# Optimization experiments

Hardware: AMD Instinct MI355X
Metric: run time of the kernel (lower is better)

## Reference

```python
import jax, jax.numpy as jnp
import numpy as np

DIM = 1024
B, TI, TJ = 8, 2048, 2048
EPS = 1e-5


def layernorm(x, g, b):
    mu = jnp.mean(x, axis=-1, keepdims=True)
    var = jnp.var(x, axis=-1, keepdims=True)
    return (x - mu) * jax.lax.rsqrt(var + EPS) * g + b


def setup_inputs() -> dict:
    key = jax.random.key(0)
    ks = jax.random.split(key, 12)
    s = 1.0 / np.sqrt(DIM)
    return {
        "target": jax.random.normal(ks[0], (B, TI, DIM), jnp.float32),
        "source_k": jax.random.normal(ks[1], (B, TJ, DIM), jnp.float32),
        "source_v": jax.random.normal(ks[2], (B, TJ, DIM), jnp.float32),
        "Wq": jax.random.uniform(ks[3], (DIM, DIM), jnp.float32, -s, s),
        "bq": jax.random.uniform(ks[4], (DIM,), jnp.float32, -s, s),
        "Wk": jax.random.uniform(ks[5], (DIM, DIM), jnp.float32, -s, s),
        "bk": jax.random.uniform(ks[6], (DIM,), jnp.float32, -s, s),
        "Wv": jax.random.uniform(ks[7], (DIM, DIM), jnp.float32, -s, s),
        "bv": jax.random.uniform(ks[8], (DIM,), jnp.float32, -s, s),
        "g_t": jnp.ones((DIM,), jnp.float32),
        "b_t": jnp.zeros((DIM,), jnp.float32),
        "g_k": jnp.ones((DIM,), jnp.float32),
        "b_k": jnp.zeros((DIM,), jnp.float32),
        "g_v": jnp.ones((DIM,), jnp.float32),
        "b_v": jnp.zeros((DIM,), jnp.float32),
    }


def reference(target, source_k, source_v, Wq, bq, Wk, bk, Wv, bv,
              g_t, b_t, g_k, b_k, g_v, b_v):
    scale = DIM ** (-0.5)
    t = layernorm(target, g_t, b_t)
    sk = layernorm(source_k, g_k, b_k)
    sv = layernorm(source_v, g_v, b_v)
    # torch Linear: x @ W.T + b
    q = jnp.einsum('bid,ed->bie', t, Wq) + bq
    k = jnp.einsum('bjd,ed->bje', sk, Wk) + bk
    v = jnp.einsum('bjd,ed->bje', sv, Wv) + bv
    dots = jnp.einsum('bid,bjd->bij', q, k) * scale
    attn = jax.nn.softmax(dots, axis=2)
    return jnp.einsum('bij,bjd->bid', attn, v)
```

## Files before the change

kernel.cpp:

```cpp
#include <hip/hip_runtime.h>
#include <cstdint>

using u16 = unsigned short;
using u32 = unsigned int;
typedef __attribute__((ext_vector_type(8))) short short8;
typedef __attribute__((ext_vector_type(4))) float f32x4;

__device__ __forceinline__ float bf2f(u16 u) { return __uint_as_float(((u32)u) << 16); }
__device__ __forceinline__ u16 f2bf(float f) {
    u32 u = __float_as_uint(f);
    u32 r = u + 0x7fffu + ((u >> 16) & 1u);
    return (u16)(r >> 16);
}

__device__ __forceinline__ void load_lds16(const void* g, void* l) {
    __builtin_amdgcn_global_load_lds((const __attribute__((address_space(1))) void*)g,
                                     (__attribute__((address_space(3))) void*)l, 16, 0, 0);
}

__global__ __launch_bounds__(256)
void ln_cast_kernel(const float* __restrict__ x, const float* __restrict__ gw,
                    const float* __restrict__ bw, u16* __restrict__ y) {
    const int row = blockIdx.x;
    const int tid = threadIdx.x;
    const float4 v = ((const float4*)(x + (size_t)row * 1024))[tid];
    float s  = v.x + v.y + v.z + v.w;
    float ss = v.x * v.x + v.y * v.y + v.z * v.z + v.w * v.w;
#pragma unroll
    for (int off = 32; off; off >>= 1) {
        s  += __shfl_xor(s, off);
        ss += __shfl_xor(ss, off);
    }
    __shared__ float sm[8];
    const int lane = tid & 63, wid = tid >> 6;
    if (lane == 0) { sm[wid] = s; sm[wid + 4] = ss; }
    __syncthreads();
    s  = sm[0] + sm[1] + sm[2] + sm[3];
    ss = sm[4] + sm[5] + sm[6] + sm[7];
    const float mu   = s * (1.0f / 1024.0f);
    const float var  = ss * (1.0f / 1024.0f) - mu * mu;
    const float rstd = rsqrtf(var + 1e-5f);
    const float4 g4 = ((const float4*)gw)[tid];
    const float4 b4 = ((const float4*)bw)[tid];
    u16 o[4];
    o[0] = f2bf((v.x - mu) * rstd * g4.x + b4.x);
    o[1] = f2bf((v.y - mu) * rstd * g4.y + b4.y);
    o[2] = f2bf((v.z - mu) * rstd * g4.z + b4.z);
    o[3] = f2bf((v.w - mu) * rstd * g4.w + b4.w);
    *(uint2*)(y + (size_t)row * 1024 + tid * 4) = *(uint2*)o;
}

__global__ __launch_bounds__(256)
void cast_kernel(const float* __restrict__ x, u16* __restrict__ y) {
    const int i = blockIdx.x * 256 + threadIdx.x;
    const float4 v = ((const float4*)x)[i];
    u16 o[4] = { f2bf(v.x), f2bf(v.y), f2bf(v.z), f2bf(v.w) };
    *(uint2*)(y + (size_t)i * 4) = *(uint2*)o;
}

template<int MODE>
__global__ __launch_bounds__(256)
void gemm_bt(const u16* __restrict__ A, const u16* __restrict__ B,
             const float* __restrict__ bias, void* __restrict__ Cout,
             const int M, const int N, const int K, const float scale,
             const long sA, const long sB, const long sC)
{
    const int bz = blockIdx.z;
    A += (long)bz * sA;
    B += (long)bz * sB;
    __shared__ __align__(16) u16 As[128 * 64];
    __shared__ __align__(16) u16 Bs[128 * 64];
    const int tid  = threadIdx.x;
    const int lane = tid & 63, wid = tid >> 6;
    const int wm = (wid & 1) * 64, wn = (wid >> 1) * 64;
    const int m0 = blockIdx.x * 128, n0 = blockIdx.y * 128;

    const int scol = (tid & 7) ^ ((tid >> 3) & 7);
    const u16* ap = A + (long)(m0 + (tid >> 3)) * K + scol * 8;
    const u16* bp = B + (long)(n0 + (tid >> 3)) * K + scol * 8;
    u16* asd = As + wid * 512;
    u16* bsd = Bs + wid * 512;
    const long rs32 = 32L * K;

    f32x4 acc[4][4] = {};
    const int fr = lane & 15, fq = lane >> 4;

    for (int k0 = 0; k0 < K; k0 += 64) {
#pragma unroll
        for (int rd = 0; rd < 4; rd++) {
            load_lds16(ap + k0 + rd * rs32, asd + rd * 2048);
            load_lds16(bp + k0 + rd * rs32, bsd + rd * 2048);
        }
        __syncthreads();
#pragma unroll
        for (int s = 0; s < 2; s++) {
            short8 af[4], bfv[4];
#pragma unroll
            for (int i = 0; i < 4; i++) {
                const int row = wm + i * 16 + fr;
                af[i] = *(const short8*)&As[row * 64 + (((s * 4 + fq) ^ (row & 7)) * 8)];
            }
#pragma unroll
            for (int j = 0; j < 4; j++) {
                const int row = wn + j * 16 + fr;
                bfv[j] = *(const short8*)&Bs[row * 64 + (((s * 4 + fq) ^ (row & 7)) * 8)];
            }
#pragma unroll
            for (int i = 0; i < 4; i++)
#pragma unroll
                for (int j = 0; j < 4; j++)
                    acc[i][j] = __builtin_amdgcn_mfma_f32_16x16x32_bf16(af[i], bfv[j], acc[i][j], 0, 0, 0);
        }
        __syncthreads();
    }

    const int cn = lane & 15;
    const int cm = (lane >> 4) * 4;
#pragma unroll
    for (int i = 0; i < 4; i++) {
        const int gmb = m0 + wm + i * 16 + cm;
#pragma unroll
        for (int j = 0; j < 4; j++) {
            const int gn = n0 + wn + j * 16 + cn;
            const float bv = (MODE <= 1) ? bias[gn] : 0.0f;
            if (MODE == 1) {
                const int batch = gmb >> 11;
                const int jj = gmb & 2047;
                u16 o[4];
#pragma unroll
                for (int r = 0; r < 4; r++) o[r] = f2bf(acc[i][j][r] + bv);
                *(uint2*)((u16*)Cout + ((long)batch * N + gn) * 2048 + jj) = *(uint2*)o;
            } else {
#pragma unroll
                for (int r = 0; r < 4; r++) {
                    const long gm = gmb + r;
                    float v = acc[i][j][r];
                    if (MODE == 0) v += bv;
                    if (MODE == 2) v *= scale;
                    if (MODE == 3)
                        ((float*)Cout)[(long)bz * sC + gm * N + gn] = v;
                    else if (MODE == 2)
                        ((u16*)Cout)[(long)bz * sC + gm * N + gn] = f2bf(v);
                    else
                        ((u16*)Cout)[gm * (long)N + gn] = f2bf(v);
                }
            }
        }
    }
}

__global__ __launch_bounds__(256)
void softmax_kernel(u16* __restrict__ S) {
    const size_t row = blockIdx.x;
    u16* r = S + row * 2048;
    const int tid = threadIdx.x;
    const uint4 raw = *(const uint4*)(r + tid * 8);
    float v[8];
    v[0] = bf2f((u16)(raw.x & 0xffffu)); v[1] = bf2f((u16)(raw.x >> 16));
    v[2] = bf2f((u16)(raw.y & 0xffffu)); v[3] = bf2f((u16)(raw.y >> 16));
    v[4] = bf2f((u16)(raw.z & 0xffffu)); v[5] = bf2f((u16)(raw.z >> 16));
    v[6] = bf2f((u16)(raw.w & 0xffffu)); v[7] = bf2f((u16)(raw.w >> 16));
    float mx = v[0];
#pragma unroll
    for (int i = 1; i < 8; i++) mx = fmaxf(mx, v[i]);
#pragma unroll
    for (int off = 32; off; off >>= 1) mx = fmaxf(mx, __shfl_xor(mx, off));
    __shared__ float sm[4];
    __shared__ float sm2[4];
    const int lane = tid & 63, wid = tid >> 6;
    if (lane == 0) sm[wid] = mx;
    __syncthreads();
    mx = fmaxf(fmaxf(sm[0], sm[1]), fmaxf(sm[2], sm[3]));
    float s = 0.f;
#pragma unroll
    for (int i = 0; i < 8; i++) { v[i] = __expf(v[i] - mx); s += v[i]; }
#pragma unroll
    for (int off = 32; off; off >>= 1) s += __shfl_xor(s, off);
    if (lane == 0) sm2[wid] = s;
    __syncthreads();
    s = sm2[0] + sm2[1] + sm2[2] + sm2[3];
    const float inv = 1.0f / s;
    u16 o[8];
#pragma unroll
    for (int i = 0; i < 8; i++) o[i] = f2bf(v[i] * inv);
    *(uint4*)(r + tid * 8) = *(uint4*)o;
}

extern "C" void kernel_launch(void* const* d_in, const int* in_sizes, int n_in,
                              void* d_out, int out_size, void* d_ws, size_t ws_size,
                              hipStream_t stream) {
    const float* target = (const float*)d_in[0];
    const float* src_k  = (const float*)d_in[1];
    const float* src_v  = (const float*)d_in[2];
    const float* Wq = (const float*)d_in[3];
    const float* bq = (const float*)d_in[4];
    const float* Wk = (const float*)d_in[5];
    const float* bk = (const float*)d_in[6];
    const float* Wv = (const float*)d_in[7];
    const float* bv = (const float*)d_in[8];
    const float* g_t = (const float*)d_in[9];
    const float* b_t = (const float*)d_in[10];
    const float* g_k = (const float*)d_in[11];
    const float* b_k = (const float*)d_in[12];
    const float* g_v = (const float*)d_in[13];
    const float* b_v = (const float*)d_in[14];

    char* ws = (char*)d_ws;
    u16* q   = (u16*)(ws + 0);
    u16* kk  = (u16*)(ws + 33554432L);
    u16* vT  = (u16*)(ws + 67108864L);
    u16* ln  = (u16*)(ws + 100663296L);
    u16* wqb = (u16*)(ws + 134217728L);
    u16* wkb = wqb + 1048576;
    u16* wvb = wkb + 1048576;
    u16* S   = (u16*)(ws + 100663296L);

    const float scale = 0.03125f;

    cast_kernel<<<1024, 256, 0, stream>>>(Wq, wqb);
    cast_kernel<<<1024, 256, 0, stream>>>(Wk, wkb);
    cast_kernel<<<1024, 256, 0, stream>>>(Wv, wvb);

    ln_cast_kernel<<<16384, 256, 0, stream>>>(target, g_t, b_t, ln);
    gemm_bt<0><<<dim3(128, 8, 1), 256, 0, stream>>>(ln, wqb, bq, q,
        16384, 1024, 1024, 1.0f, 0, 0, 0);
    ln_cast_kernel<<<16384, 256, 0, stream>>>(src_k, g_k, b_k, ln);
    gemm_bt<0><<<dim3(128, 8, 1), 256, 0, stream>>>(ln, wkb, bk, kk,
        16384, 1024, 1024, 1.0f, 0, 0, 0);
    ln_cast_kernel<<<16384, 256, 0, stream>>>(src_v, g_v, b_v, ln);
    gemm_bt<1><<<dim3(128, 8, 1), 256, 0, stream>>>(ln, wvb, bv, vT,
        16384, 1024, 1024, 1.0f, 0, 0, 0);

    gemm_bt<2><<<dim3(16, 16, 8), 256, 0, stream>>>(q, kk, nullptr, S,
        2048, 2048, 1024, scale, 2048L * 1024, 2048L * 1024, 2048L * 2048);

    softmax_kernel<<<16384, 256, 0, stream>>>(S);

    gemm_bt<3><<<dim3(16, 8, 8), 256, 0, stream>>>(S, vT, nullptr, d_out,
        2048, 1024, 2048, 1.0f, 2048L * 2048, 1024L * 2048, 2048L * 1024);
}
```

Before: 602.9 us.

## Fuse softmax into attention GEMMs via exp epilogue and MFMA row sums

```diff
diff --git a/kernel.cpp b/kernel.cpp
--- a/kernel.cpp
+++ b/kernel.cpp
@@ -51,15 +51,20 @@
 }
 
 __global__ __launch_bounds__(256)
-void cast_kernel(const float* __restrict__ x, u16* __restrict__ y) {
-    const int i = blockIdx.x * 256 + threadIdx.x;
-    const float4 v = ((const float4*)x)[i];
+void cast3_kernel(const float* __restrict__ wa, const float* __restrict__ wb,
+                  const float* __restrict__ wc, u16* __restrict__ oa) {
+    const int bid = blockIdx.x;
+    const int sel = bid >> 10;
+    const float* s = (sel == 0) ? wa : (sel == 1) ? wb : wc;
+    u16* d = oa + (size_t)sel * 1048576;
+    const int i = (bid & 1023) * 256 + threadIdx.x;
+    const float4 v = ((const float4*)s)[i];
     u16 o[4] = { f2bf(v.x), f2bf(v.y), f2bf(v.z), f2bf(v.w) };
-    *(uint2*)(y + (size_t)i * 4) = *(uint2*)o;
+    *(uint2*)(d + (size_t)i * 4) = *(uint2*)o;
 }
 
 template<int MODE>
-__global__ __launch_bounds__(256)
+__global__ __launch_bounds__(256, (MODE == 3 ? 3 : 4))
 void gemm_bt(const u16* __restrict__ A, const u16* __restrict__ B,
              const float* __restrict__ bias, void* __restrict__ Cout,
              const int M, const int N, const int K, const float scale,
@@ -83,6 +88,8 @@
     const long rs32 = 32L * K;
 
     f32x4 acc[4][4] = {};
+    f32x4 acc_l[4] = {};
+    const short8 ones8 = {16256, 16256, 16256, 16256, 16256, 16256, 16256, 16256};
     const int fr = lane & 15, fq = lane >> 4;
 
     for (int k0 = 0; k0 < K; k0 += 64) {
@@ -110,12 +117,24 @@
 #pragma unroll
                 for (int j = 0; j < 4; j++)
                     acc[i][j] = __builtin_amdgcn_mfma_f32_16x16x32_bf16(af[i], bfv[j], acc[i][j], 0, 0, 0);
+            if (MODE == 3) {
+#pragma unroll
+                for (int i = 0; i < 4; i++)
+                    acc_l[i] = __builtin_amdgcn_mfma_f32_16x16x32_bf16(af[i], ones8, acc_l[i], 0, 0, 0);
+            }
         }
         __syncthreads();
     }
 
     const int cn = lane & 15;
     const int cm = (lane >> 4) * 4;
+    float invl[4][4];
+    if (MODE == 3) {
+#pragma unroll
+        for (int i = 0; i < 4; i++)
+#pragma unroll
+            for (int r = 0; r < 4; r++) invl[i][r] = 1.0f / acc_l[i][r];
+    }
 #pragma unroll
     for (int i = 0; i < 4; i++) {
         const int gmb = m0 + wm + i * 16 + cm;
@@ -136,9 +155,9 @@
                     const long gm = gmb + r;
                     float v = acc[i][j][r];
                     if (MODE == 0) v += bv;
-                    if (MODE == 2) v *= scale;
+                    if (MODE == 2) v = __expf(v * scale);
                     if (MODE == 3)
-                        ((float*)Cout)[(long)bz * sC + gm * N + gn] = v;
+                        ((float*)Cout)[(long)bz * sC + gm * N + gn] = v * invl[i][r];
                     else if (MODE == 2)
                         ((u16*)Cout)[(long)bz * sC + gm * N + gn] = f2bf(v);
                     else
@@ -147,43 +166,6 @@
             }
         }
     }
-}
-
-__global__ __launch_bounds__(256)
-void softmax_kernel(u16* __restrict__ S) {
-    const size_t row = blockIdx.x;
-    u16* r = S + row * 2048;
-    const int tid = threadIdx.x;
-    const uint4 raw = *(const uint4*)(r + tid * 8);
-    float v[8];
-    v[0] = bf2f((u16)(raw.x & 0xffffu)); v[1] = bf2f((u16)(raw.x >> 16));
-    v[2] = bf2f((u16)(raw.y & 0xffffu)); v[3] = bf2f((u16)(raw.y >> 16));
-    v[4] = bf2f((u16)(raw.z & 0xffffu)); v[5] = bf2f((u16)(raw.z >> 16));
-    v[6] = bf2f((u16)(raw.w & 0xffffu)); v[7] = bf2f((u16)(raw.w >> 16));
-    float mx = v[0];
-#pragma unroll
-    for (int i = 1; i < 8; i++) mx = fmaxf(mx, v[i]);
-#pragma unroll
-    for (int off = 32; off; off >>= 1) mx = fmaxf(mx, __shfl_xor(mx, off));
-    __shared__ float sm[4];
-    __shared__ float sm2[4];
-    const int lane = tid & 63, wid = tid >> 6;
-    if (lane == 0) sm[wid] = mx;
-    __syncthreads();
-    mx = fmaxf(fmaxf(sm[0], sm[1]), fmaxf(sm[2], sm[3]));
-    float s = 0.f;
-#pragma unroll
-    for (int i = 0; i < 8; i++) { v[i] = __expf(v[i] - mx); s += v[i]; }
-#pragma unroll
-    for (int off = 32; off; off >>= 1) s += __shfl_xor(s, off);
-    if (lane == 0) sm2[wid] = s;
-    __syncthreads();
-    s = sm2[0] + sm2[1] + sm2[2] + sm2[3];
-    const float inv = 1.0f / s;
-    u16 o[8];
-#pragma unroll
-    for (int i = 0; i < 8; i++) o[i] = f2bf(v[i] * inv);
-    *(uint4*)(r + tid * 8) = *(uint4*)o;
 }
 
 extern "C" void kernel_launch(void* const* d_in, const int* in_sizes, int n_in,
@@ -217,9 +199,7 @@
 
     const float scale = 0.03125f;
 
-    cast_kernel<<<1024, 256, 0, stream>>>(Wq, wqb);
-    cast_kernel<<<1024, 256, 0, stream>>>(Wk, wkb);
-    cast_kernel<<<1024, 256, 0, stream>>>(Wv, wvb);
+    cast3_kernel<<<3072, 256, 0, stream>>>(Wq, Wk, Wv, wqb);
 
     ln_cast_kernel<<<16384, 256, 0, stream>>>(target, g_t, b_t, ln);
     gemm_bt<0><<<dim3(128, 8, 1), 256, 0, stream>>>(ln, wqb, bq, q,
@@ -234,8 +214,6 @@
     gemm_bt<2><<<dim3(16, 16, 8), 256, 0, stream>>>(q, kk, nullptr, S,
         2048, 2048, 1024, scale, 2048L * 1024, 2048L * 1024, 2048L * 2048);
 
-    softmax_kernel<<<16384, 256, 0, stream>>>(S);
-
     gemm_bt<3><<<dim3(16, 8, 8), 256, 0, stream>>>(S, vT, nullptr, d_out,
         2048, 1024, 2048, 1.0f, 2048L * 2048, 1024L * 2048, 2048L * 1024);
 }
```

Result: faster. 534.5 us (-11.3%).
